# Optimization experiments

Hardware: AMD Instinct MI355X
Metric: run time of the kernel (lower is better)

Reference implementation:

```python
import jax, jax.numpy as jnp
import numpy as np

N, D, V = 4096, 2048, 50257
IGNORE_INDEX = -100


def setup_inputs() -> dict:
    key = jax.random.key(0)
    k1, k2, k3 = jax.random.split(key, 3)
    x = jax.random.normal(k1, (N, D), dtype=jnp.float32)
    # lm_head.weight is [V, D]; the fused op receives weight.T -> [D, V]
    weight = jax.random.normal(k2, (D, V), dtype=jnp.float32) * (1.0 / np.sqrt(D))
    target = jax.random.randint(k3, (N,), 0, V, dtype=jnp.int64)
    return {"x": x, "weight": weight, "target": target}


def reference(x, weight, target):
    # Fused linear + cross-entropy (reduction='sum'), matching the Helion kernel math:
    # logits accumulated in fp32, online logsumexp == plain stable logsumexp.
    logits = jnp.matmul(x, weight, preferred_element_type=jnp.float32)  # [N, V] fp32
    lse = jax.nn.logsumexp(logits, axis=-1)                              # [N]
    tgt_idx = jnp.clip(target, 0, V - 1)                                 # safe gather
    target_logits = jnp.take_along_axis(logits, tgt_idx[:, None], axis=-1)[:, 0]
    per_token_loss = lse - target_logits                                 # [N]
    mask = (target != IGNORE_INDEX).astype(per_token_loss.dtype)
    ce_loss = jnp.sum(per_token_loss * mask)                             # reduction='sum'
    return ce_loss
```

## Files before the change

kernel.cpp:

```cpp
#include <hip/hip_runtime.h>
#include <hip/hip_bf16.h>
#include <stdint.h>

#define N_TOK 4096
#define DDIM  2048
#define VOCAB 50257
#define IGNORE_INDEX (-100)

#define BM 128
#define BN 128
#define BK 64
#define NT (DDIM / BK)
#define VCHUNKS ((VOCAB + BN - 1) / BN)
#define VP (VCHUNKS * BN)
#define ROW_TILES (N_TOK / BM)
#define GRID_MAIN (VCHUNKS * ROW_TILES)

#define W_SCALE 32.0f
#define W_INV   0.03125f
#define SCALE_1 0x7F7F7F7FU

typedef float f32x4  __attribute__((ext_vector_type(4)));
typedef float f32x16 __attribute__((ext_vector_type(16)));
typedef int   i32x4  __attribute__((ext_vector_type(4)));
typedef int   i32x8  __attribute__((ext_vector_type(8)));

__device__ __forceinline__ uint32_t pack2bf(float a, float b) {
  uint32_t ua = __float_as_uint(a);
  uint32_t ub = __float_as_uint(b);
  uint32_t ra = (ua + 0x7fffu + ((ua >> 16) & 1u)) >> 16;
  uint32_t rb = (ub + 0x7fffu + ((ub >> 16) & 1u)) & 0xffff0000u;
  return (ra & 0xffffu) | rb;
}

__device__ __forceinline__ uint32_t f32_to_e4m3(float f) {
  uint32_t u = __float_as_uint(f);
  uint32_t s = (u >> 24) & 0x80u;
  float a = fabsf(f);
  if (a >= 448.f) return s | 0x7Eu;
  if (a >= 0.015625f) {
    uint32_t m = __float_as_uint(a);
    m += 0x7FFFFu + ((m >> 20) & 1u);
    uint32_t e = (m >> 23) - 120u;
    return s | (e << 3) | ((m >> 20) & 7u);
  }
  uint32_t m = (uint32_t)rintf(a * 512.f);
  return s | m;
}

__device__ __forceinline__ void gload_lds16(const void* g, void* l) {
  __builtin_amdgcn_global_load_lds(
      (const __attribute__((address_space(1))) uint32_t*)g,
      (__attribute__((address_space(3))) uint32_t*)l, 16, 0, 0);
}

__global__ __launch_bounds__(256) void convert_x8(const float* __restrict__ x,
                                                  uint8_t* __restrict__ x8) {
  int t = blockIdx.x * 256 + threadIdx.x;
  const float4* xp = (const float4*)x + (size_t)t * 4;
  uint32_t u[4];
  #pragma unroll
  for (int g = 0; g < 4; ++g) {
    float4 f = xp[g];
    u[g] = f32_to_e4m3(f.x) | (f32_to_e4m3(f.y) << 8) |
           (f32_to_e4m3(f.z) << 16) | (f32_to_e4m3(f.w) << 24);
  }
  ((uint4*)x8)[t] = make_uint4(u[0], u[1], u[2], u[3]);
}

__global__ __launch_bounds__(256) void transpose_w8(const float* __restrict__ w,
                                                    uint8_t* __restrict__ w8) {
  __shared__ float t[64][65];
  const int vb = blockIdx.x * 64;
  const int kb = blockIdx.y * 64;
  const int tid = threadIdx.x;
  const int tv = tid & 63, tk4 = tid >> 6;
  #pragma unroll
  for (int i = 0; i < 16; ++i) {
    int kl = tk4 + i * 4;
    int v = vb + tv;
    t[kl][tv] = (v < VOCAB) ? w[(size_t)(kb + kl) * VOCAB + v] * W_SCALE : 0.f;
  }
  __syncthreads();
  const int vl = tid >> 2, seg = tid & 3;
  uint32_t u[4];
  #pragma unroll
  for (int g = 0; g < 4; ++g) {
    u[g] = 0;
    #pragma unroll
    for (int j = 0; j < 4; ++j)
      u[g] |= f32_to_e4m3(t[seg * 16 + g * 4 + j][vl]) << (8 * j);
  }
  *(uint4*)(w8 + (size_t)(vb + vl) * DDIM + kb + seg * 16) =
      make_uint4(u[0], u[1], u[2], u[3]);
}

__global__ __launch_bounds__(256, 3) void lmhead_main(
    const uint8_t* __restrict__ w8, const uint8_t* __restrict__ x8,
    const int* __restrict__ tgt,
    float2* __restrict__ partial, float* __restrict__ tlogit)
{
  __shared__ char lds[32768];
  __shared__ float2 stats[2][BM];

  const int bid = blockIdx.x;
  const int v = bid >> 5;
  const int r = bid & 31;
  const int v0 = v * BN;
  const int m0 = r * BM;
  const int tid = threadIdx.x;
  const int lane = tid & 63;
  const int wid = tid >> 6;
  const int wn = wid >> 1, wm = wid & 1;

  f32x16 acc[2][2];
  #pragma unroll
  for (int i = 0; i < 2; ++i)
    #pragma unroll
    for (int j = 0; j < 2; ++j) acc[i][j] = (f32x16)0.f;

  const int jj = lane >> 3;
  const int lu_s = (lane & 7) ^ jj;
  const int srow = 2 * jj + (lu_s >> 2);
  const int sk = (lu_s & 3) * 16;
  const uint8_t* wsrc = w8 + (size_t)(v0 + srow) * DDIM + sk;
  const uint8_t* xsrc = x8 + (size_t)(m0 + srow) * DDIM + sk;

  const int r5 = lane & 31, hi = lane >> 5;
  const int j7 = (r5 >> 1) & 7;
  const int lu0 = ((r5 & 1) << 2) | (hi << 1);
  const int rdoff = (r5 >> 1) * 128 + ((lu0 ^ j7) << 4);
  const int aoff0 = wn * 32 * 128 + rdoff;
  const int boff0 = wm * 32 * 128 + rdoff;

  auto stage = [&](int T) {
    char* Al = lds + (T & 1) * 16384;
    char* Bl = Al + 8192;
    const size_t ko = (size_t)T * BK;
    #pragma unroll
    for (int i = 0; i < 2; ++i) {
      int c = wid * 2 + i;
      gload_lds16(wsrc + (size_t)c * 16 * DDIM + ko, Al + c * 1024);
      gload_lds16(xsrc + (size_t)c * 16 * DDIM + ko, Bl + c * 1024);
    }
  };

  stage(0);
  __syncthreads();

  for (int t = 0; t < NT; ++t) {
    if (t + 1 < NT) stage(t + 1);
    const char* Al = lds + (t & 1) * 16384;
    const char* Bl = Al + 8192;
    i32x8 bv[2];
    #pragma unroll
    for (int bj = 0; bj < 2; ++bj) {
      i32x4 b0 = *(const i32x4*)(Bl + boff0 + bj * 2048);
      i32x4 b1 = *(const i32x4*)(Bl + (boff0 ^ 16) + bj * 2048);
      bv[bj] = __builtin_shufflevector(b0, b1, 0, 1, 2, 3, 4, 5, 6, 7);
    }
    #pragma unroll
    for (int bi = 0; bi < 2; ++bi) {
      i32x4 a0 = *(const i32x4*)(Al + aoff0 + bi * 2048);
      i32x4 a1 = *(const i32x4*)(Al + (aoff0 ^ 16) + bi * 2048);
      i32x8 av = __builtin_shufflevector(a0, a1, 0, 1, 2, 3, 4, 5, 6, 7);
      #pragma unroll
      for (int bj = 0; bj < 2; ++bj)
        acc[bi][bj] = __builtin_amdgcn_mfma_scale_f32_32x32x64_f8f6f4(
            av, bv[bj], acc[bi][bj], 0 , 0 ,
            0, SCALE_1, 0, SCALE_1);
    }
    __syncthreads();
  }

  #pragma unroll
  for (int bj = 0; bj < 2; ++bj) {
    const int m_g = m0 + wm * 64 + bj * 32 + r5;
    float vmax = -INFINITY;
    #pragma unroll
    for (int bi = 0; bi < 2; ++bi) {
      #pragma unroll
      for (int rg = 0; rg < 16; ++rg) {
        int n_g = v0 + wn * 64 + bi * 32 + (rg & 3) + 8 * (rg >> 2) + 4 * hi;
        if (n_g < VOCAB) vmax = fmaxf(vmax, acc[bi][bj][rg] * W_INV);
      }
    }
    vmax = fmaxf(vmax, __shfl_xor(vmax, 32, 64));
    float ssum = 0.f;
    const int t = tgt[m_g];
    #pragma unroll
    for (int bi = 0; bi < 2; ++bi) {
      #pragma unroll
      for (int rg = 0; rg < 16; ++rg) {
        int n_g = v0 + wn * 64 + bi * 32 + (rg & 3) + 8 * (rg >> 2) + 4 * hi;
        float val = acc[bi][bj][rg] * W_INV;
        if (n_g < VOCAB) ssum += __expf(val - vmax);
        if (n_g == t) tlogit[m_g] = val;
      }
    }
    ssum += __shfl_xor(ssum, 32, 64);
    if (hi == 0) stats[wn][wm * 64 + bj * 32 + r5] = make_float2(vmax, ssum);
  }
  __syncthreads();
  if (tid < BM) {
    float2 a = stats[0][tid], b = stats[1][tid];
    float M = fmaxf(a.x, b.x);
    float S = a.y * __expf(a.x - M) + b.y * __expf(b.x - M);
    partial[(size_t)(m0 + tid) * VCHUNKS + v] = make_float2(M, S);
  }
}

typedef short bf16x8 __attribute__((ext_vector_type(8)));

__global__ __launch_bounds__(256, 2) void lmhead_partial_fb(
    const float* __restrict__ x, const float* __restrict__ w,
    const int* __restrict__ tgt,
    float2* __restrict__ partial, float* __restrict__ tlogit)
{
  __shared__ uint4 xs[BM * 64 * 2 / 16];
  __shared__ uint4 wtl[BN * 64 * 2 / 16];
  __shared__ float2 stats[2][BM];

  const int bid = blockIdx.x;
  const int v = bid >> 5;
  const int r = bid & 31;
  const int v0 = v * BN;
  const int m0 = r * BM;
  const int tid = threadIdx.x;
  const int lane = tid & 63;
  const int wid = tid >> 6;
  const int wn = wid >> 1, wm = wid & 1;
  const int lr = lane & 15, lk = lane >> 4;

  f32x4 acc[4][4];
  #pragma unroll
  for (int i = 0; i < 4; ++i)
    #pragma unroll
    for (int j = 0; j < 4; ++j) acc[i][j] = (f32x4)0.f;

  char* xsb = (char*)xs;
  char* wtb = (char*)wtl;

  for (int kt = 0; kt < DDIM / 64; ++kt) {
    const int k0 = kt * 64;
    __syncthreads();
    #pragma unroll
    for (int i = 0; i < 4; ++i) {
      int t = tid + i * 256;
      int m = t >> 3, kg = t & 7;
      const float* gp = x + (size_t)(m0 + m) * DDIM + k0 + kg * 8;
      float4 f0 = *(const float4*)gp;
      float4 f1 = *(const float4*)(gp + 4);
      uint4 pk;
      pk.x = pack2bf(f0.x, f0.y); pk.y = pack2bf(f0.z, f0.w);
      pk.z = pack2bf(f1.x, f1.y); pk.w = pack2bf(f1.z, f1.w);
      int byte = (m * 128 + kg * 16) ^ ((m & 7) << 4);
      *(uint4*)(xsb + byte) = pk;
    }
    #pragma unroll
    for (int i = 0; i < 4; ++i) {
      int t = tid + i * 256;
      int n = t & 127, kg = t >> 7;
      int col = v0 + n;
      float f[8];
      if (col < VOCAB) {
        const float* gp = w + (size_t)(k0 + kg * 8) * VOCAB + col;
        #pragma unroll
        for (int kk = 0; kk < 8; ++kk) f[kk] = gp[(size_t)kk * VOCAB];
      } else {
        #pragma unroll
        for (int kk = 0; kk < 8; ++kk) f[kk] = 0.f;
      }
      uint4 pk;
      pk.x = pack2bf(f[0], f[1]); pk.y = pack2bf(f[2], f[3]);
      pk.z = pack2bf(f[4], f[5]); pk.w = pack2bf(f[6], f[7]);
      int byte = (n * 128 + kg * 16) ^ ((n & 7) << 4);
      *(uint4*)(wtb + byte) = pk;
    }
    __syncthreads();
    #pragma unroll
    for (int ks = 0; ks < 2; ++ks) {
      bf16x8 af[4], bfr[4];
      #pragma unroll
      for (int bi = 0; bi < 4; ++bi) {
        int row = wn * 64 + bi * 16 + lr;
        int byte = (row * 128 + ks * 64 + lk * 16) ^ ((row & 7) << 4);
        af[bi] = *(const bf16x8*)(wtb + byte);
      }
      #pragma unroll
      for (int bj = 0; bj < 4; ++bj) {
        int row = wm * 64 + bj * 16 + lr;
        int byte = (row * 128 + ks * 64 + lk * 16) ^ ((row & 7) << 4);
        bfr[bj] = *(const bf16x8*)(xsb + byte);
      }
      #pragma unroll
      for (int bi = 0; bi < 4; ++bi)
        #pragma unroll
        for (int bj = 0; bj < 4; ++bj)
          acc[bi][bj] = __builtin_amdgcn_mfma_f32_16x16x32_bf16(
              af[bi], bfr[bj], acc[bi][bj], 0, 0, 0);
    }
  }

  #pragma unroll
  for (int bj = 0; bj < 4; ++bj) {
    const int m_g = m0 + wm * 64 + bj * 16 + lr;
    float vmax = -INFINITY;
    #pragma unroll
    for (int bi = 0; bi < 4; ++bi)
      #pragma unroll
      for (int rg = 0; rg < 4; ++rg) {
        int n_g = v0 + wn * 64 + bi * 16 + lk * 4 + rg;
        if (n_g < VOCAB) vmax = fmaxf(vmax, acc[bi][bj][rg]);
      }
    vmax = fmaxf(vmax, __shfl_xor(vmax, 16, 64));
    vmax = fmaxf(vmax, __shfl_xor(vmax, 32, 64));
    float ssum = 0.f;
    const int t = tgt[m_g];
    #pragma unroll
    for (int bi = 0; bi < 4; ++bi)
      #pragma unroll
      for (int rg = 0; rg < 4; ++rg) {
        int n_g = v0 + wn * 64 + bi * 16 + lk * 4 + rg;
        float val = acc[bi][bj][rg];
        if (n_g < VOCAB) ssum += __expf(val - vmax);
        if (n_g == t) tlogit[m_g] = val;
      }
    ssum += __shfl_xor(ssum, 16, 64);
    ssum += __shfl_xor(ssum, 32, 64);
    if (lk == 0) stats[wn][wm * 64 + bj * 16 + lr] = make_float2(vmax, ssum);
  }
  __syncthreads();
  if (tid < BM) {
    float2 a = stats[0][tid], b = stats[1][tid];
    float M = fmaxf(a.x, b.x);
    float S = a.y * __expf(a.x - M) + b.y * __expf(b.x - M);
    partial[(size_t)(m0 + tid) * VCHUNKS + v] = make_float2(M, S);
  }
}

__device__ __forceinline__ void lse_merge(float& m, float& s, float M, float S) {
  if (S > 0.f) {
    if (M > m) { s = s * __expf(m - M) + S; m = M; }
    else       { s += S * __expf(M - m); }
  }
}

__global__ void lmhead_reduce(const float2* __restrict__ partial,
                              const float* __restrict__ tlogit,
                              const int* __restrict__ tgt,
                              float* __restrict__ out)
{
  const int wid = threadIdx.x >> 6;
  const int lane = threadIdx.x & 63;
  const int row = blockIdx.x * 4 + wid;
  float m = -INFINITY, s = 0.f;
  for (int c = lane; c < VCHUNKS; c += 64) {
    float2 p = partial[(size_t)row * VCHUNKS + c];
    lse_merge(m, s, p.x, p.y);
  }
  #pragma unroll
  for (int off = 1; off < 64; off <<= 1) {
    float M = __shfl_xor(m, off, 64);
    float S = __shfl_xor(s, off, 64);
    lse_merge(m, s, M, S);
  }
  if (lane == 0) {
    int t = tgt[row];
    if (t != IGNORE_INDEX) {
      float loss = m + __logf(s) - tlogit[row];
      atomicAdd(out, loss);
    }
  }
}

extern "C" void kernel_launch(void* const* d_in, const int* in_sizes, int n_in,
                              void* d_out, int out_size, void* d_ws, size_t ws_size,
                              hipStream_t stream) {
  const float* x = (const float*)d_in[0];
  const float* w = (const float*)d_in[1];
  const int* tgt = (const int*)d_in[2];
  float* out = (float*)d_out;

  const size_t w8_bytes = (size_t)VP * DDIM;
  const size_t x8_bytes = (size_t)N_TOK * DDIM;
  const size_t part_bytes = (size_t)N_TOK * VCHUNKS * 8;
  const size_t tl_bytes = (size_t)N_TOK * 4;
  const size_t need = w8_bytes + x8_bytes + part_bytes + tl_bytes;

  hipMemsetAsync(d_out, 0, sizeof(float), stream);

  if (ws_size >= need) {
    uint8_t* w8 = (uint8_t*)d_ws;
    uint8_t* x8 = (uint8_t*)d_ws + w8_bytes;
    float2* partial = (float2*)((char*)d_ws + w8_bytes + x8_bytes);
    float* tlogit = (float*)((char*)d_ws + w8_bytes + x8_bytes + part_bytes);

    convert_x8<<<dim3(N_TOK * DDIM / 16 / 256), 256, 0, stream>>>(x, x8);
    transpose_w8<<<dim3(VP / 64, DDIM / 64), 256, 0, stream>>>(w, w8);
    lmhead_main<<<dim3(GRID_MAIN), 256, 0, stream>>>(w8, x8, tgt, partial, tlogit);
    lmhead_reduce<<<dim3(N_TOK / 4), 256, 0, stream>>>(partial, tlogit, tgt, out);
  } else {
    float2* partial = (float2*)d_ws;
    float* tlogit = (float*)((char*)d_ws + part_bytes);
    lmhead_partial_fb<<<dim3(GRID_MAIN), 256, 0, stream>>>(x, w, tgt, partial, tlogit);
    lmhead_reduce<<<dim3(N_TOK / 4), 256, 0, stream>>>(partial, tlogit, tgt, out);
  }
}
```

Baseline: 718.9 us.

## Load x tile directly into registers, keep only weight tile in LDS

The x (B operand) tile is now read straight from global memory into registers in the MFMA fragment layout, double-buffered in registers, and no longer staged through LDS. LDS shrinks to a double-buffered weight tile only. The goal is to cut LDS traffic and footprint, which could allow more occupancy. In exchange, global loads for x are issued per wave with less coalescing, different waves redundantly fetch the same x rows, and register pressure rises.

```diff
diff --git a/kernel.cpp b/kernel.cpp
--- a/kernel.cpp
+++ b/kernel.cpp
@@ -95,12 +95,14 @@
       make_uint4(u[0], u[1], u[2], u[3]);
 }
 
+struct Bregs { i32x4 v[2][2]; };
+
 __global__ __launch_bounds__(256, 3) void lmhead_main(
     const uint8_t* __restrict__ w8, const uint8_t* __restrict__ x8,
     const int* __restrict__ tgt,
     float2* __restrict__ partial, float* __restrict__ tlogit)
 {
-  __shared__ char lds[32768];
+  __shared__ char lds[16384];
   __shared__ float2 stats[2][BM];
 
   const int bid = blockIdx.x;
@@ -124,45 +126,42 @@
   const int srow = 2 * jj + (lu_s >> 2);
   const int sk = (lu_s & 3) * 16;
   const uint8_t* wsrc = w8 + (size_t)(v0 + srow) * DDIM + sk;
-  const uint8_t* xsrc = x8 + (size_t)(m0 + srow) * DDIM + sk;
 
   const int r5 = lane & 31, hi = lane >> 5;
   const int j7 = (r5 >> 1) & 7;
   const int lu0 = ((r5 & 1) << 2) | (hi << 1);
   const int rdoff = (r5 >> 1) * 128 + ((lu0 ^ j7) << 4);
-  const int aoff0 = wn * 32 * 128 + rdoff;
-  const int boff0 = wm * 32 * 128 + rdoff;
-
-  auto stage = [&](int T) {
-    char* Al = lds + (T & 1) * 16384;
-    char* Bl = Al + 8192;
+  const int aoff0 = wn * 4096 + rdoff;
+
+  const uint8_t* xbase = x8 + (size_t)(m0 + wm * 64 + r5) * DDIM + hi * 32;
+
+  auto stageA = [&](int T, int s) {
+    char* Al = lds + s * 8192;
     const size_t ko = (size_t)T * BK;
     #pragma unroll
     for (int i = 0; i < 2; ++i) {
       int c = wid * 2 + i;
       gload_lds16(wsrc + (size_t)c * 16 * DDIM + ko, Al + c * 1024);
-      gload_lds16(xsrc + (size_t)c * 16 * DDIM + ko, Bl + c * 1024);
     }
   };
-
-  stage(0);
-  __syncthreads();
-
-  for (int t = 0; t < NT; ++t) {
-    if (t + 1 < NT) stage(t + 1);
-    const char* Al = lds + (t & 1) * 16384;
-    const char* Bl = Al + 8192;
+  auto loadB = [&](Bregs& B, int T) {
+    const uint8_t* p = xbase + (size_t)T * BK;
+    #pragma unroll
+    for (int bj = 0; bj < 2; ++bj)
+      #pragma unroll
+      for (int c = 0; c < 2; ++c)
+        B.v[bj][c] = *(const i32x4*)(p + (size_t)bj * 32 * DDIM + c * 16);
+  };
+  auto computeT = [&](const char* Al, const Bregs& B) {
     i32x8 bv[2];
     #pragma unroll
-    for (int bj = 0; bj < 2; ++bj) {
-      i32x4 b0 = *(const i32x4*)(Bl + boff0 + bj * 2048);
-      i32x4 b1 = *(const i32x4*)(Bl + (boff0 ^ 16) + bj * 2048);
-      bv[bj] = __builtin_shufflevector(b0, b1, 0, 1, 2, 3, 4, 5, 6, 7);
-    }
+    for (int bj = 0; bj < 2; ++bj)
+      bv[bj] = __builtin_shufflevector(B.v[bj][0], B.v[bj][1],
+                                       0, 1, 2, 3, 4, 5, 6, 7);
     #pragma unroll
     for (int bi = 0; bi < 2; ++bi) {
-      i32x4 a0 = *(const i32x4*)(Al + aoff0 + bi * 2048);
-      i32x4 a1 = *(const i32x4*)(Al + (aoff0 ^ 16) + bi * 2048);
+      i32x4 a0 = *(const i32x4*)(Al + (aoff0 + bi * 2048));
+      i32x4 a1 = *(const i32x4*)(Al + ((aoff0 ^ 16) + bi * 2048));
       i32x8 av = __builtin_shufflevector(a0, a1, 0, 1, 2, 3, 4, 5, 6, 7);
       #pragma unroll
       for (int bj = 0; bj < 2; ++bj)
@@ -170,6 +169,19 @@
             av, bv[bj], acc[bi][bj], 0 , 0 ,
             0, SCALE_1, 0, SCALE_1);
     }
+  };
+
+  Bregs B0, B1;
+  stageA(0, 0);
+  loadB(B0, 0);
+  __syncthreads();
+
+  for (int t = 0; t < NT; t += 2) {
+    if (t + 1 < NT) { stageA(t + 1, 1); loadB(B1, t + 1); }
+    computeT(lds, B0);
+    __syncthreads();
+    if (t + 2 < NT) { stageA(t + 2, 0); loadB(B0, t + 2); }
+    computeT(lds + 8192, B1);
     __syncthreads();
   }
 
```

Measured after the change: 1.046 ms. +45.5%, slower.
